# Kernel tuning notes

Hardware: AMD Instinct MI355X
Metric: run time of the kernel (lower is better)

Reference implementation:

```python
import jax, jax.numpy as jnp
import numpy as np

LOG2 = float(np.log(2.0))
N_NODES = 100000

def ssp(x):
    return jax.nn.softplus(x) - LOG2

def _xavier(key, out_dim, in_dim):
    bound = float(np.sqrt(6.0 / (in_dim + out_dim)))
    return jax.random.uniform(key, (out_dim, in_dim), jnp.float32, -bound, bound)

def setup_inputs() -> dict:
    key = jax.random.key(0)
    ks = jax.random.split(key, 10)
    H, F = 128, 128  # hidden_channels, num_filters
    C2 = int(2 * H * 0.5)          # lin2 out = 128
    C2h = int(2 * H) - C2          # lin2_hull out = 128
    E, Eh = 1600000, 400000
    v = jax.random.normal(ks[0], (N_NODES, H), jnp.float32)
    e = jax.random.normal(ks[1], (E, F), jnp.float32)
    edge_index = jax.random.randint(ks[2], (2, E), 0, N_NODES, jnp.int64)
    e_hull = jax.random.normal(ks[3], (Eh, F), jnp.float32)
    edge_index_hull = jax.random.randint(ks[4], (2, Eh), 0, N_NODES, jnp.int64)
    return {
        "v": v, "e": e, "edge_index": edge_index,
        "e_hull": e_hull, "edge_index_hull": edge_index_hull,
        "W1": _xavier(ks[5], H, F), "b1": jnp.zeros((H,), jnp.float32),
        "W2": _xavier(ks[6], C2, H), "b2": jnp.zeros((C2,), jnp.float32),
        "W1h": _xavier(ks[7], H, F), "b1h": jnp.zeros((H,), jnp.float32),
        "W2h": _xavier(ks[8], C2h, H), "b2h": jnp.zeros((C2h,), jnp.float32),
        "Wc": _xavier(ks[9], H, C2 + C2h), "bc": jnp.zeros((H,), jnp.float32),
    }

def reference(v, e, edge_index, e_hull, edge_index_hull,
              W1, b1, W2, b2, W1h, b1h, W2h, b2h, Wc, bc):
    n = v.shape[0]
    i = edge_index[1]
    out = jax.ops.segment_sum(e, i, num_segments=n)          # [N, F] scatter-sum
    out = ssp(out @ W1.T + b1) @ W2.T + b2                   # [N, C2]
    i_ = edge_index_hull[1]
    out_hull = jax.ops.segment_sum(e_hull, i_, num_segments=n)
    out_hull = ssp(out_hull @ W1h.T + b1h) @ W2h.T + b2h     # [N, C2h]
    cat = jnp.concatenate([out, out_hull], axis=1)           # [N, C2+C2h]
    return v + ssp(cat @ Wc.T + bc)
```

## Files before the change

kernel.cpp:

```cpp
#include <hip/hip_runtime.h>
#include <math.h>

typedef __attribute__((ext_vector_type(8))) short short8;
typedef __attribute__((ext_vector_type(4))) float f32x4;
typedef unsigned short u16;
typedef unsigned int u32;

#define PADM 64
#define PADH 32

__device__ __forceinline__ float ssp(float x) {
    const float LOG2E = 1.44269504088896340736f;
    const float LN2   = 0.69314718055994530942f;
    float t = __builtin_amdgcn_exp2f(-fabsf(x) * LOG2E);
    return fmaxf(x, 0.0f) + LN2 * __builtin_amdgcn_logf(1.0f + t) - LN2;
}

__device__ __forceinline__ u16 f2bf(float x) {
    u32 u = __float_as_uint(x);
    u32 r = (u + 0x7FFFu + ((u >> 16) & 1u)) >> 16;
    return (u16)r;
}

__global__ __launch_bounds__(256) void place_pad_kernel(
    const int* __restrict__ tgt_m, int E,
    const int* __restrict__ tgt_h, int Eh,
    int* __restrict__ cursors, int* __restrict__ perm, int N,
    const float* __restrict__ W1, const float* __restrict__ W1h,
    const float* __restrict__ W2, const float* __restrict__ W2h,
    const float* __restrict__ Wc, u16* __restrict__ Wbf)
{
    int i = blockIdx.x * 256 + threadIdx.x;
    if (i < E) {
        int node = tgt_m[i];
        int pos = atomicAdd(&cursors[node], 1);
        if (pos < PADM)
            __builtin_nontemporal_store(i, &perm[node * PADM + pos]);
    } else if (i < E + Eh) {
        int node = tgt_h[i - E];
        int pos = atomicAdd(&cursors[N + node], 1);
        if (pos < PADH)
            __builtin_nontemporal_store(i - E, &perm[(size_t)N * PADM + node * PADH + pos]);
    } else {
        int j = i - (E + Eh);
        if (j < 98304) {
            const float* src; int off;
            if      (j < 16384) { src = W1;  off = j; }
            else if (j < 32768) { src = W1h; off = j - 16384; }
            else if (j < 49152) { src = W2;  off = j - 32768; }
            else if (j < 65536) { src = W2h; off = j - 49152; }
            else                { src = Wc;  off = j - 65536; }
            Wbf[j] = f2bf(src[off]);
        }
    }
}

__device__ __forceinline__ f32x4 gather_rows(
    const f32x4* __restrict__ src, const int* __restrict__ seg,
    int cnt, int c4)
{
    f32x4 s = {0.f, 0.f, 0.f, 0.f};
    int k = 0;
    for (; k + 8 <= cnt; k += 8) {
        int p[8];
        #pragma unroll
        for (int q = 0; q < 8; q++) p[q] = seg[k + q];
        f32x4 r[8];
        #pragma unroll
        for (int q = 0; q < 8; q++)
            r[q] = __builtin_nontemporal_load(&src[(size_t)p[q] * 32 + c4]);
        s += ((r[0] + r[1]) + (r[2] + r[3])) + ((r[4] + r[5]) + (r[6] + r[7]));
    }
    if (k + 4 <= cnt) {
        int p0 = seg[k], p1 = seg[k + 1], p2 = seg[k + 2], p3 = seg[k + 3];
        f32x4 a = __builtin_nontemporal_load(&src[(size_t)p0 * 32 + c4]);
        f32x4 b = __builtin_nontemporal_load(&src[(size_t)p1 * 32 + c4]);
        f32x4 c = __builtin_nontemporal_load(&src[(size_t)p2 * 32 + c4]);
        f32x4 d = __builtin_nontemporal_load(&src[(size_t)p3 * 32 + c4]);
        s += (a + b) + (c + d);
        k += 4;
    }
    for (; k + 2 <= cnt; k += 2) {
        int p0 = seg[k], p1 = seg[k + 1];
        s += __builtin_nontemporal_load(&src[(size_t)p0 * 32 + c4])
           + __builtin_nontemporal_load(&src[(size_t)p1 * 32 + c4]);
    }
    if (k < cnt)
        s += __builtin_nontemporal_load(&src[(size_t)seg[k] * 32 + c4]);
    return s;
}

#define MT 64

#define CHUNK_IDX(row, ch) (((row) * 16 + ((ch) ^ ((row) & 7))))
#define AFRAG(ls, row, ch) (*(const short8*)&(ls)[CHUNK_IDX(row, ch) * 8])

__device__ __forceinline__ void layer128(
    u16* __restrict__ ls, const u16* __restrict__ W,
    const float* __restrict__ bias,
    int rw, int lr, int kc, bool act)
{
    const int arow = rw + lr;
    short8 af[4];
    #pragma unroll
    for (int s = 0; s < 4; s++) af[s] = AFRAG(ls, arow, s * 4 + kc);
    #pragma unroll
    for (int nt = 0; nt < 8; nt++) {
        const int bcol = nt * 16 + lr;
        const short8* wr = (const short8*)(W + bcol * 128);
        f32x4 acc = {0.f, 0.f, 0.f, 0.f};
        #pragma unroll
        for (int s = 0; s < 4; s++)
            acc = __builtin_amdgcn_mfma_f32_16x16x32_bf16(af[s], wr[s * 4 + kc], acc, 0, 0, 0);
        const float bn = bias[bcol];
        #pragma unroll
        for (int r = 0; r < 4; r++) {
            const int drow = rw + kc * 4 + r;
            float val = acc[r] + bn;
            if (act) val = ssp(val);
            ls[CHUNK_IDX(drow, bcol >> 3) * 8 + (bcol & 7)] = f2bf(val);
        }
    }
}

__global__ __launch_bounds__(256, 5) void fused_mlp_kernel(
    const float* __restrict__ e, const float* __restrict__ eh,
    const int* __restrict__ perm, const int* __restrict__ cursors,
    const u16* __restrict__ Wbf,
    const float* __restrict__ b1, const float* __restrict__ b1h,
    const float* __restrict__ b2, const float* __restrict__ b2h,
    const float* __restrict__ bc,
    const float* __restrict__ v, float* __restrict__ out, int n)
{
    __shared__ __align__(16) u16 X0[MT * 128];
    __shared__ __align__(16) u16 X1[MT * 128];

    const int tid = threadIdx.x;
    const int l   = tid & 63;
    const int w   = tid >> 6;
    const int rw  = w * 16;
    const int lr  = l & 15;
    const int kc  = l >> 4;
    const int node0 = blockIdx.x * MT;

    const u16* W1  = Wbf;
    const u16* W1h = Wbf + 16384;
    const u16* W2  = Wbf + 32768;
    const u16* W2h = Wbf + 49152;
    const u16* Wc  = Wbf + 65536;

    const int hw = l >> 5;
    const int c4 = l & 31;
    const int ch = c4 >> 1;
    const int hf = (c4 & 1) * 4;
    for (int j = hw; j < 16; j += 2) {
        const int row  = rw + j;
        const int node = node0 + row;
        f32x4 sm = {0.f, 0.f, 0.f, 0.f};
        f32x4 sh = {0.f, 0.f, 0.f, 0.f};
        if (node < n) {
            int degm = cursors[node];         if (degm > PADM) degm = PADM;
            int degh = cursors[n + node];     if (degh > PADH) degh = PADH;
            sm = gather_rows((const f32x4*)e,  perm + (size_t)node * PADM, degm, c4);
            sh = gather_rows((const f32x4*)eh, perm + (size_t)n * PADM + (size_t)node * PADH, degh, c4);
        }
        ushort4 om, oh;
        om.x = f2bf(sm.x); om.y = f2bf(sm.y); om.z = f2bf(sm.z); om.w = f2bf(sm.w);
        oh.x = f2bf(sh.x); oh.y = f2bf(sh.y); oh.z = f2bf(sh.z); oh.w = f2bf(sh.w);
        *(ushort4*)&X0[CHUNK_IDX(row, ch) * 8 + hf] = om;
        *(ushort4*)&X1[CHUNK_IDX(row, ch) * 8 + hf] = oh;
    }

    layer128(X0, W1,  b1,  rw, lr, kc, true);
    layer128(X1, W1h, b1h, rw, lr, kc, true);
    layer128(X0, W2,  b2,  rw, lr, kc, false);
    layer128(X1, W2h, b2h, rw, lr, kc, false);

    {
        const int arow = rw + lr;
        short8 af[8];
        #pragma unroll
        for (int s = 0; s < 4; s++) af[s]     = AFRAG(X0, arow, s * 4 + kc);
        #pragma unroll
        for (int s = 0; s < 4; s++) af[s + 4] = AFRAG(X1, arow, s * 4 + kc);
        #pragma unroll
        for (int nt = 0; nt < 8; nt++) {
            const int bcol = nt * 16 + lr;
            const short8* wr = (const short8*)(Wc + bcol * 256);
            f32x4 acc = {0.f, 0.f, 0.f, 0.f};
            #pragma unroll
            for (int s = 0; s < 8; s++)
                acc = __builtin_amdgcn_mfma_f32_16x16x32_bf16(af[s], wr[s * 4 + kc], acc, 0, 0, 0);
            const float bn = bc[bcol];
            #pragma unroll
            for (int r = 0; r < 4; r++) {
                const int drow = rw + kc * 4 + r;
                const int node = node0 + drow;
                if (node < n) {
                    size_t off = (size_t)node * 128 + bcol;
                    float vv = __builtin_nontemporal_load(&v[off]);
                    __builtin_nontemporal_store(vv + ssp(acc[r] + bn), &out[off]);
                }
            }
        }
    }
}

extern "C" void kernel_launch(void* const* d_in, const int* in_sizes, int n_in,
                              void* d_out, int out_size, void* d_ws, size_t ws_size,
                              hipStream_t stream)
{
    const float* v    = (const float*)d_in[0];
    const float* e    = (const float*)d_in[1];
    const int*   ei   = (const int*)  d_in[2];
    const float* eh   = (const float*)d_in[3];
    const int*   eih  = (const int*)  d_in[4];
    const float* W1   = (const float*)d_in[5];
    const float* b1   = (const float*)d_in[6];
    const float* W2   = (const float*)d_in[7];
    const float* b2   = (const float*)d_in[8];
    const float* W1h  = (const float*)d_in[9];
    const float* b1h  = (const float*)d_in[10];
    const float* W2h  = (const float*)d_in[11];
    const float* b2h  = (const float*)d_in[12];
    const float* Wc   = (const float*)d_in[13];
    const float* bc   = (const float*)d_in[14];
    float* out = (float*)d_out;

    const int N  = in_sizes[0] / 128;
    const int E  = (int)(in_sizes[1] / 128);
    const int Eh = (int)(in_sizes[3] / 128);
    const int n2 = 2 * N;

    u16* Wbf     = (u16*)d_ws;
    int* cursors = (int*)(Wbf + 98304);
    int* perm    = cursors + n2;

    const int* tgt_m = ei  + E;
    const int* tgt_h = eih + Eh;

    const int total = E + Eh + 98304;

    (void)hipMemsetAsync(cursors, 0, (size_t)n2 * 4, stream);
    place_pad_kernel<<<(total + 255) / 256, 256, 0, stream>>>(
        tgt_m, E, tgt_h, Eh, cursors, perm, N, W1, W1h, W2, W2h, Wc, Wbf);
    fused_mlp_kernel<<<(N + MT - 1) / MT, 256, 0, stream>>>(
        e, eh, perm, cursors, Wbf, b1, b1h, b2, b2h, bc, v, out, N);
}
```

Before: 582.2 us.

## Split gather into standalone high-occupancy kernel writing bf16 intermediates

```diff
diff --git a/kernel.cpp b/kernel.cpp
--- a/kernel.cpp
+++ b/kernel.cpp
@@ -5,6 +5,7 @@
 typedef __attribute__((ext_vector_type(4))) float f32x4;
 typedef unsigned short u16;
 typedef unsigned int u32;
+typedef __attribute__((ext_vector_type(4))) u16 u16x4;
 
 #define PADM 64
 #define PADH 32
@@ -90,6 +91,39 @@
     return s;
 }
 
+__global__ __launch_bounds__(512, 8) void gather_pad_kernel(
+    const float* __restrict__ e, const float* __restrict__ eh,
+    const int* __restrict__ perm, const int* __restrict__ cursors,
+    u16* __restrict__ accm, u16* __restrict__ acch, int n)
+{
+    int slot = blockIdx.x * 16 + (threadIdx.x >> 5);
+    if (slot >= 2 * n) return;
+    const int c4 = threadIdx.x & 31;
+
+    const f32x4* src;
+    const int* seg;
+    int deg, node;
+    u16* dst;
+    if (slot < n) {
+        node = slot;
+        src  = (const f32x4*)e;
+        seg  = perm + (size_t)node * PADM;
+        deg  = cursors[slot];      if (deg > PADM) deg = PADM;
+        dst  = accm;
+    } else {
+        node = slot - n;
+        src  = (const f32x4*)eh;
+        seg  = perm + (size_t)n * PADM + (size_t)node * PADH;
+        deg  = cursors[slot];      if (deg > PADH) deg = PADH;
+        dst  = acch;
+    }
+
+    f32x4 s = gather_rows(src, seg, deg, c4);
+    u16x4 o;
+    o.x = f2bf(s.x); o.y = f2bf(s.y); o.z = f2bf(s.z); o.w = f2bf(s.w);
+    __builtin_nontemporal_store(o, (u16x4*)&dst[(size_t)node * 128 + c4 * 4]);
+}
+
 #define MT 64
 
 #define CHUNK_IDX(row, ch) (((row) * 16 + ((ch) ^ ((row) & 7))))
@@ -123,9 +157,8 @@
     }
 }
 
-__global__ __launch_bounds__(256, 5) void fused_mlp_kernel(
-    const float* __restrict__ e, const float* __restrict__ eh,
-    const int* __restrict__ perm, const int* __restrict__ cursors,
+__global__ __launch_bounds__(256, 4) void mlp_kernel(
+    const u16* __restrict__ accm, const u16* __restrict__ acch,
     const u16* __restrict__ Wbf,
     const float* __restrict__ b1, const float* __restrict__ b1h,
     const float* __restrict__ b2, const float* __restrict__ b2h,
@@ -149,26 +182,17 @@
     const u16* W2h = Wbf + 49152;
     const u16* Wc  = Wbf + 65536;
 
-    const int hw = l >> 5;
-    const int c4 = l & 31;
-    const int ch = c4 >> 1;
-    const int hf = (c4 & 1) * 4;
-    for (int j = hw; j < 16; j += 2) {
-        const int row  = rw + j;
+    for (int j = l; j < 256; j += 64) {
+        const int row = rw + (j >> 4);
+        const int c   = j & 15;
+        int4 a = make_int4(0, 0, 0, 0), b = a;
         const int node = node0 + row;
-        f32x4 sm = {0.f, 0.f, 0.f, 0.f};
-        f32x4 sh = {0.f, 0.f, 0.f, 0.f};
         if (node < n) {
-            int degm = cursors[node];         if (degm > PADM) degm = PADM;
-            int degh = cursors[n + node];     if (degh > PADH) degh = PADH;
-            sm = gather_rows((const f32x4*)e,  perm + (size_t)node * PADM, degm, c4);
-            sh = gather_rows((const f32x4*)eh, perm + (size_t)n * PADM + (size_t)node * PADH, degh, c4);
-        }
-        ushort4 om, oh;
-        om.x = f2bf(sm.x); om.y = f2bf(sm.y); om.z = f2bf(sm.z); om.w = f2bf(sm.w);
-        oh.x = f2bf(sh.x); oh.y = f2bf(sh.y); oh.z = f2bf(sh.z); oh.w = f2bf(sh.w);
-        *(ushort4*)&X0[CHUNK_IDX(row, ch) * 8 + hf] = om;
-        *(ushort4*)&X1[CHUNK_IDX(row, ch) * 8 + hf] = oh;
+            a = ((const int4*)accm)[(size_t)node * 16 + c];
+            b = ((const int4*)acch)[(size_t)node * 16 + c];
+        }
+        ((int4*)X0)[CHUNK_IDX(row, c)] = a;
+        ((int4*)X1)[CHUNK_IDX(row, c)] = b;
     }
 
     layer128(X0, W1,  b1,  rw, lr, kc, true);
@@ -233,7 +257,9 @@
     const int n2 = 2 * N;
 
     u16* Wbf     = (u16*)d_ws;
-    int* cursors = (int*)(Wbf + 98304);
+    u16* accm    = Wbf + 98304;
+    u16* acch    = accm + (size_t)N * 128;
+    int* cursors = (int*)(acch + (size_t)N * 128);
     int* perm    = cursors + n2;
 
     const int* tgt_m = ei  + E;
@@ -244,6 +270,8 @@
     (void)hipMemsetAsync(cursors, 0, (size_t)n2 * 4, stream);
     place_pad_kernel<<<(total + 255) / 256, 256, 0, stream>>>(
         tgt_m, E, tgt_h, Eh, cursors, perm, N, W1, W1h, W2, W2h, Wc, Wbf);
-    fused_mlp_kernel<<<(N + MT - 1) / MT, 256, 0, stream>>>(
-        e, eh, perm, cursors, Wbf, b1, b1h, b2, b2h, bc, v, out, N);
-}
+    gather_pad_kernel<<<(n2 + 15) / 16, 512, 0, stream>>>(
+        e, eh, perm, cursors, accm, acch, N);
+    mlp_kernel<<<(N + MT - 1) / MT, 256, 0, stream>>>(
+        accm, acch, Wbf, b1, b1h, b2, b2h, bc, v, out, N);
+}
```

After: 592.4 us. No clear change (+1.7%).
